# Performance work log

Hardware: AMD Instinct MI355X
Metric: run time of the kernel (lower is better)

## Reference

```python
import jax, jax.numpy as jnp
import numpy as np

N_ATOMS = 100000   # real atoms (index 0 is padding row -> total rows N_ATOMS+1)
N_BONDS = 200000   # real directed bonds (index 0 is padding row)
MAX_NB = 6
HIDDEN = 300
ATOM_FDIM = 133
BOND_FDIM = 147
DEPTH = 3
N_MOLS = 5000
ATOMS_PER_MOL = N_ATOMS // N_MOLS


def setup_inputs() -> dict:
    key = jax.random.key(0)
    ks = jax.random.split(key, 8)
    f_atoms = jax.random.normal(ks[0], (N_ATOMS + 1, ATOM_FDIM), dtype=jnp.float32)
    f_atoms = f_atoms.at[0].set(0.0)  # chemprop zero-padding row
    f_bonds = jax.random.normal(ks[1], (N_BONDS + 1, BOND_FDIM), dtype=jnp.float32)
    f_bonds = f_bonds.at[0].set(0.0)
    # weights (Linear stored as [in, out]); bias=False for W_i/W_h, W_o has bias
    W_i = jax.random.normal(ks[2], (BOND_FDIM, HIDDEN), dtype=jnp.float32) * 0.05
    W_h = jax.random.normal(ks[3], (HIDDEN, HIDDEN), dtype=jnp.float32) * 0.05
    W_o = jax.random.normal(ks[4], (ATOM_FDIM + HIDDEN, HIDDEN), dtype=jnp.float32) * 0.05
    b_o = jnp.zeros((HIDDEN,), dtype=jnp.float32)
    # a2b: incoming bond ids per atom, padded with 0 (padding row of message is 0)
    a2b = jax.random.randint(ks[5], (N_ATOMS + 1, MAX_NB), 0, N_BONDS + 1, dtype=jnp.int32)
    a2b = a2b.at[0].set(0)
    # b2a: source atom of each bond
    b2a = jax.random.randint(ks[6], (N_BONDS + 1,), 1, N_ATOMS + 1, dtype=jnp.int32)
    b2a = b2a.at[0].set(0)
    # b2revb: reverse-bond pairing; bonds (2k+1, 2k+2) are partners, 0 -> 0
    idx = jnp.arange(N_BONDS + 1, dtype=jnp.int32)
    b2revb = jnp.where(idx == 0, 0, ((idx - 1) ^ 1) + 1).astype(jnp.int32)
    # molecule segment id for each real atom (replaces a_scope loop)
    mol_ids = (jnp.arange(N_ATOMS, dtype=jnp.int32) // ATOMS_PER_MOL).astype(jnp.int32)
    return {"f_atoms": f_atoms, "f_bonds": f_bonds, "W_i": W_i, "W_h": W_h,
            "W_o": W_o, "b_o": b_o, "a2b": a2b, "b2a": b2a, "b2revb": b2revb,
            "mol_ids": mol_ids}


def reference(f_atoms, f_bonds, W_i, W_h, W_o, b_o, a2b, b2a, b2revb, mol_ids):
    # input = act(W_i(f_bonds))  (ReLU, bias=False)
    inp = jax.nn.relu(f_bonds @ W_i)                    # [B+1, H]
    message = inp
    for _ in range(DEPTH - 1):
        nei = message[a2b]                              # [A+1, MAX_NB, H] gather
        a_message = nei.sum(axis=1)                     # [A+1, H]
        message = a_message[b2a] - message[b2revb]      # [B+1, H]
        message = jax.nn.relu(inp + message @ W_h)      # skip-connection + act
    # final atom readout
    a_message = message[a2b].sum(axis=1)                # [A+1, H]
    a_input = jnp.concatenate([f_atoms, a_message], axis=1)
    atom_hiddens = jax.nn.relu(a_input @ W_o + b_o)     # [A+1, H]
    # per-molecule mean pooling over real atoms (rows 1:)
    real = atom_hiddens[1:]                             # [A, H]
    sums = jax.ops.segment_sum(real, mol_ids, num_segments=N_MOLS)
    counts = jax.ops.segment_sum(jnp.ones((N_ATOMS,), dtype=real.dtype), mol_ids,
                                 num_segments=N_MOLS)
    mol_vecs = sums / jnp.maximum(counts, 1.0)[:, None]  # [N_MOLS, H]
    return mol_vecs
```

## Files before the change

### kernel.cpp

```cpp
#include <hip/hip_runtime.h>
#include <hip/hip_bf16.h>

#define N_ATOMS   100000
#define N_BONDS   200000
#define MAX_NB    6
#define HIDDEN    300
#define ATOM_FDIM 133
#define BOND_FDIM 147
#define N_MOLS    5000
#define APM       20

#define MB_ROWS (N_BONDS + 1)
#define MA_ROWS (N_ATOMS + 1)

#define CHUNKS_B 1280
#define EPS      308

typedef unsigned short bf16_t;
typedef __attribute__((ext_vector_type(8))) __bf16 bf16x8;
typedef __attribute__((ext_vector_type(4))) float  float4v;

__device__ __forceinline__ float bf2f(unsigned short u) {
    union { unsigned int i; float f; } x; x.i = ((unsigned int)u) << 16; return x.f;
}
__device__ __forceinline__ unsigned short f2bf(float f) {
    union { float f; unsigned int i; } x; x.f = f;
    unsigned int r = x.i + 0x7FFFu + ((x.i >> 16) & 1u);
    return (unsigned short)(r >> 16);
}

__global__ __launch_bounds__(256) void prep_w(
    const float* __restrict__ W, bf16_t* __restrict__ dst, int K, int total_chunks)
{
    int idx = blockIdx.x * 256 + threadIdx.x;
    if (idx >= total_chunks) return;
    int kb  = idx / CHUNKS_B;
    int c   = idx - kb * CHUNKS_B;
    int cq  = c / 320;
    int col = c - cq * 320;
    unsigned short v[8];
    #pragma unroll
    for (int j = 0; j < 8; ++j) {
        int k = kb * 32 + cq * 8 + j;
        float f = (k < K && col < HIDDEN) ? W[(size_t)k * HIDDEN + col] : 0.f;
        v[j] = f2bf(f);
    }
    bf16_t* p = dst + (size_t)idx * 8;
    *(ushort4*)(p)     = make_ushort4(v[0], v[1], v[2], v[3]);
    *(ushort4*)(p + 4) = make_ushort4(v[4], v[5], v[6], v[7]);
}

template<int MODE, int KB>
__global__ __launch_bounds__(512, 4) void gemm_mfma(
    const float* __restrict__ Af,
    const bf16_t* __restrict__ Ab1, const bf16_t* __restrict__ Ab2,
    const int* __restrict__ b2a, const int* __restrict__ b2revb,
    const bf16_t* __restrict__ WB, const float* __restrict__ bias,
    const bf16_t* __restrict__ addend, bf16_t* __restrict__ Y,
    int M)
{
    const int S = HIDDEN;
    constexpr int QG = KB * 4;
    constexpr int LDS_BYTES = (KB * 4096 > 16 * EPS * 4) ? KB * 4096 : 16 * EPS * 4;
    __shared__ __align__(16) char lds_pool[LDS_BYTES];
    bf16_t* As  = (bf16_t*)lds_pool;
    float*  epi = (float*)lds_pool;
    __shared__ int rowmap[128];

    const int tid  = threadIdx.x;
    const int lane = tid & 63;
    const int w    = tid >> 6;
    const int wm   = w >> 2;
    const int wn   = w & 3;
    const int lrow = lane & 15;
    const int q    = lane >> 4;
    const int bm   = blockIdx.x * 64;

    if (MODE == 1) {
        if (tid < 64) {
            int sr = bm + tid;
            rowmap[tid] = (sr < M) ? b2a[sr] : 0;
        } else if (tid < 128) {
            int sr = bm + tid - 64;
            rowmap[tid] = (sr < M) ? b2revb[sr] : 0;
        }
        __syncthreads();
    }

    for (int t = tid; t < 64 * QG; t += 512) {
        int row = t / QG;
        int qg  = t - row * QG;
        int k0  = qg * 8;
        unsigned short av[8];
        if (MODE == 1) {
            const bf16_t* pa = Ab1 + (size_t)rowmap[row]      * S;
            const bf16_t* pc = Ab2 + (size_t)rowmap[64 + row] * S;
            if (k0 + 8 <= S) {
                ushort4 a0 = *(const ushort4*)(pa + k0);
                ushort4 a1 = *(const ushort4*)(pa + k0 + 4);
                ushort4 c0 = *(const ushort4*)(pc + k0);
                ushort4 c1 = *(const ushort4*)(pc + k0 + 4);
                av[0] = f2bf(bf2f(a0.x) - bf2f(c0.x));
                av[1] = f2bf(bf2f(a0.y) - bf2f(c0.y));
                av[2] = f2bf(bf2f(a0.z) - bf2f(c0.z));
                av[3] = f2bf(bf2f(a0.w) - bf2f(c0.w));
                av[4] = f2bf(bf2f(a1.x) - bf2f(c1.x));
                av[5] = f2bf(bf2f(a1.y) - bf2f(c1.y));
                av[6] = f2bf(bf2f(a1.z) - bf2f(c1.z));
                av[7] = f2bf(bf2f(a1.w) - bf2f(c1.w));
            } else {
                #pragma unroll
                for (int j = 0; j < 8; ++j) {
                    int k = k0 + j;
                    av[j] = (k < S) ? f2bf(bf2f(pa[k]) - bf2f(pc[k]))
                                    : (unsigned short)0;
                }
            }
        } else if (MODE == 0) {
            int srow = bm + row;
            #pragma unroll
            for (int j = 0; j < 8; ++j) {
                int k = k0 + j;
                av[j] = (srow < M && k < BOND_FDIM)
                        ? f2bf(Af[(size_t)srow * BOND_FDIM + k]) : (unsigned short)0;
            }
        } else {
            int srow = bm + row;
            #pragma unroll
            for (int j = 0; j < 8; ++j) {
                int k = k0 + j;
                unsigned short u = 0;
                if (srow < M) {
                    if (k < ATOM_FDIM)
                        u = f2bf(Af[(size_t)srow * ATOM_FDIM + k]);
                    else if (k < ATOM_FDIM + HIDDEN)
                        u = Ab1[(size_t)srow * S + (k - ATOM_FDIM)];
                }
                av[j] = u;
            }
        }
        bf16_t* dst = As + (size_t)(qg * 64 + row) * 8;
        *(ushort4*)(dst)     = make_ushort4(av[0], av[1], av[2], av[3]);
        *(ushort4*)(dst + 4) = make_ushort4(av[4], av[5], av[6], av[7]);
    }

    float4v acc[2][5];
    #pragma unroll
    for (int i = 0; i < 2; ++i)
        #pragma unroll
        for (int j = 0; j < 5; ++j) {
            float4v z = {0.f, 0.f, 0.f, 0.f};
            acc[i][j] = z;
        }

    __syncthreads();

    const bf16_t* wbase = WB + (size_t)(q * 320 + wn * 80 + lrow) * 8;
    #pragma unroll 2
    for (int kb = 0; kb < KB; ++kb) {
        bf16x8 af0 = *(const bf16x8*)(As + (size_t)((kb * 4 + q) * 64 + wm * 32 + lrow) * 8);
        bf16x8 af1 = *(const bf16x8*)(As + (size_t)((kb * 4 + q) * 64 + wm * 32 + 16 + lrow) * 8);
        const bf16_t* wk = wbase + (size_t)kb * (CHUNKS_B * 8);
        #pragma unroll
        for (int nt = 0; nt < 5; ++nt) {
            const int c0 = wn * 80 + nt * 16;
            if (c0 < HIDDEN) {
                bf16x8 bfr = *(const bf16x8*)(wk + (size_t)nt * 16 * 8);
                acc[0][nt] = __builtin_amdgcn_mfma_f32_16x16x32_bf16(af0, bfr, acc[0][nt], 0, 0, 0);
                acc[1][nt] = __builtin_amdgcn_mfma_f32_16x16x32_bf16(af1, bfr, acc[1][nt], 0, 0, 0);
            }
        }
    }

    __syncthreads();
    #pragma unroll
    for (int mt = 0; mt < 2; ++mt) {
        for (int wh = 0; wh < 2; ++wh) {
            if (wm == wh) {
                #pragma unroll
                for (int nt = 0; nt < 5; ++nt) {
                    const int c0 = wn * 80 + nt * 16;
                    if (c0 < HIDDEN) {
                        #pragma unroll
                        for (int r = 0; r < 4; ++r)
                            epi[(q * 4 + r) * EPS + c0 + lrow] = acc[mt][nt][r];
                    }
                }
            }
            __syncthreads();
            const int row0 = bm + wh * 32 + mt * 16;
            for (int s = tid; s < 16 * 75; s += 512) {
                int rr = s / 75;
                int c4 = s - rr * 75;
                int grow = row0 + rr;
                if (grow < M) {
                    float4 v = *(const float4*)&epi[rr * EPS + c4 * 4];
                    if (MODE == 1) {
                        ushort4 ad = *(const ushort4*)(addend + (size_t)grow * S + c4 * 4);
                        v.x += bf2f(ad.x); v.y += bf2f(ad.y);
                        v.z += bf2f(ad.z); v.w += bf2f(ad.w);
                    }
                    if (MODE == 2) {
                        float4 bv = *(const float4*)(bias + c4 * 4);
                        v.x += bv.x; v.y += bv.y; v.z += bv.z; v.w += bv.w;
                    }
                    ushort4 o;
                    o.x = f2bf(v.x > 0.f ? v.x : 0.f);
                    o.y = f2bf(v.y > 0.f ? v.y : 0.f);
                    o.z = f2bf(v.z > 0.f ? v.z : 0.f);
                    o.w = f2bf(v.w > 0.f ? v.w : 0.f);
                    *(ushort4*)(Y + (size_t)grow * S + c4 * 4) = o;
                }
            }
            __syncthreads();
        }
    }
}


__global__ __launch_bounds__(256) void aggregate_k(
    const bf16_t* __restrict__ msg, const int* __restrict__ a2b,
    bf16_t* __restrict__ amsg)
{
    int idx = blockIdx.x * blockDim.x + threadIdx.x;
    const int total = MA_ROWS * 75;
    if (idx >= total) return;
    int a  = idx / 75;
    int c4 = idx - a * 75;
    const int* nb = a2b + (size_t)a * MAX_NB;
    float4 s = make_float4(0.f, 0.f, 0.f, 0.f);
    #pragma unroll
    for (int j = 0; j < MAX_NB; ++j) {
        int b = nb[j];
        ushort4 u = *(const ushort4*)(msg + (size_t)b * HIDDEN + c4 * 4);
        s.x += bf2f(u.x); s.y += bf2f(u.y); s.z += bf2f(u.z); s.w += bf2f(u.w);
    }
    ushort4 o;
    o.x = f2bf(s.x); o.y = f2bf(s.y); o.z = f2bf(s.z); o.w = f2bf(s.w);
    *(ushort4*)(amsg + (size_t)a * HIDDEN + c4 * 4) = o;
}

__global__ __launch_bounds__(256) void mol_mean_k(
    const bf16_t* __restrict__ atom_h, float* __restrict__ out)
{
    int idx = blockIdx.x * blockDim.x + threadIdx.x;
    if (idx >= N_MOLS * 75) return;
    int m  = idx / 75;
    int c4 = idx - m * 75;
    const bf16_t* base = atom_h + (size_t)(1 + m * APM) * HIDDEN + c4 * 4;
    float4 s = make_float4(0.f, 0.f, 0.f, 0.f);
    #pragma unroll
    for (int i = 0; i < APM; ++i) {
        ushort4 u = *(const ushort4*)(base + (size_t)i * HIDDEN);
        s.x += bf2f(u.x); s.y += bf2f(u.y); s.z += bf2f(u.z); s.w += bf2f(u.w);
    }
    const float inv = 1.0f / (float)APM;
    s.x *= inv; s.y *= inv; s.z *= inv; s.w *= inv;
    *(float4*)(out + (size_t)m * HIDDEN + c4 * 4) = s;
}

extern "C" void kernel_launch(void* const* d_in, const int* in_sizes, int n_in,
                              void* d_out, int out_size, void* d_ws, size_t ws_size,
                              hipStream_t stream)
{
    const float* f_atoms = (const float*)d_in[0];
    const float* f_bonds = (const float*)d_in[1];
    const float* W_i     = (const float*)d_in[2];
    const float* W_h     = (const float*)d_in[3];
    const float* W_o     = (const float*)d_in[4];
    const float* b_o     = (const float*)d_in[5];
    const int*   a2b     = (const int*)d_in[6];
    const int*   b2a     = (const int*)d_in[7];
    const int*   b2revb  = (const int*)d_in[8];
    float* out = (float*)d_out;

    char* base = (char*)d_ws;
    const size_t SZ_BOND_B = (((size_t)MB_ROWS * HIDDEN * sizeof(bf16_t)) + 255) & ~(size_t)255;
    bf16_t* inp  = (bf16_t*)(base);
    bf16_t* msgA = (bf16_t*)(base + SZ_BOND_B);
    bf16_t* amsg = (bf16_t*)(base + 2 * SZ_BOND_B);

    char* scratch = (char*)d_out;
    bf16_t* Wib = (bf16_t*)(scratch);
    bf16_t* Whb = (bf16_t*)(scratch + 102400);
    bf16_t* Wob = (bf16_t*)(scratch + 307200);

    dim3 blk512(512), blk256(256);
    const int gb = (MB_ROWS + 63) / 64;
    const int ga = (MA_ROWS + 63) / 64;
    int agg_blocks  = (MA_ROWS * 75 + 255) / 256;
    int mean_blocks = (N_MOLS * 75 + 255) / 256;

    prep_w<<<(5  * CHUNKS_B + 255) / 256, blk256, 0, stream>>>(W_i, Wib, BOND_FDIM, 5 * CHUNKS_B);
    prep_w<<<(10 * CHUNKS_B + 255) / 256, blk256, 0, stream>>>(W_h, Whb, HIDDEN, 10 * CHUNKS_B);
    prep_w<<<(14 * CHUNKS_B + 255) / 256, blk256, 0, stream>>>(W_o, Wob, ATOM_FDIM + HIDDEN, 14 * CHUNKS_B);

    gemm_mfma<0, 5><<<gb, blk512, 0, stream>>>(
        f_bonds, nullptr, nullptr, nullptr, nullptr,
        Wib, nullptr, nullptr, inp, MB_ROWS);

    aggregate_k<<<agg_blocks, blk256, 0, stream>>>(inp, a2b, amsg);
    gemm_mfma<1, 10><<<gb, blk512, 0, stream>>>(
        nullptr, amsg, inp, b2a, b2revb,
        Whb, nullptr, inp, msgA, MB_ROWS);

    aggregate_k<<<agg_blocks, blk256, 0, stream>>>(msgA, a2b, amsg);
    gemm_mfma<1, 10><<<gb, blk512, 0, stream>>>(
        nullptr, amsg, msgA, b2a, b2revb,
        Whb, nullptr, inp, inp, MB_ROWS);

    aggregate_k<<<agg_blocks, blk256, 0, stream>>>(inp, a2b, amsg);
    gemm_mfma<2, 14><<<ga, blk512, 0, stream>>>(
        f_atoms, amsg, nullptr, nullptr, nullptr,
        Wob, b_o, nullptr, msgA, MA_ROWS);

    mol_mean_k<<<mean_blocks, blk256, 0, stream>>>(msgA, out);
}
```

Before: 947.1 us.

## Batch gathers, pad LDS rows, prefetch weight fragments, widen aggregate per thread

The A-tile staging now issues all global loads into registers before converting and storing them to LDS, so more gathers are in flight at once. LDS rows are padded to 65 to cut bank conflicts. The MFMA loop is fully unrolled and double-buffers the B fragments from global memory. W_o is K-permuted so atom features align to 136, which lets the readout GEMM load message columns as vector chunks. The aggregate kernel now handles 12 columns per thread with all neighbor loads issued up front. The price is higher register pressure under launch_bounds(512,4), which could cause spills.

```diff
diff --git a/kernel.cpp b/kernel.cpp
--- a/kernel.cpp
+++ b/kernel.cpp
@@ -15,6 +15,7 @@
 
 #define CHUNKS_B 1280
 #define EPS      308
+#define ROWP     65
 
 typedef unsigned short bf16_t;
 typedef __attribute__((ext_vector_type(8))) __bf16 bf16x8;
@@ -30,7 +31,8 @@
 }
 
 __global__ __launch_bounds__(256) void prep_w(
-    const float* __restrict__ W, bf16_t* __restrict__ dst, int K, int total_chunks)
+    const float* __restrict__ W, bf16_t* __restrict__ dst, int K,
+    int total_chunks, int perm)
 {
     int idx = blockIdx.x * 256 + threadIdx.x;
     if (idx >= total_chunks) return;
@@ -42,7 +44,10 @@
     #pragma unroll
     for (int j = 0; j < 8; ++j) {
         int k = kb * 32 + cq * 8 + j;
-        float f = (k < K && col < HIDDEN) ? W[(size_t)k * HIDDEN + col] : 0.f;
+        int ksrc;
+        if (perm) ksrc = (k < 133) ? k : ((k >= 136 && k < 436) ? k - 3 : -1);
+        else      ksrc = (k < K) ? k : -1;
+        float f = (ksrc >= 0 && col < HIDDEN) ? W[(size_t)ksrc * HIDDEN + col] : 0.f;
         v[j] = f2bf(f);
     }
     bf16_t* p = dst + (size_t)idx * 8;
@@ -61,7 +66,9 @@
 {
     const int S = HIDDEN;
     constexpr int QG = KB * 4;
-    constexpr int LDS_BYTES = (KB * 4096 > 16 * EPS * 4) ? KB * 4096 : 16 * EPS * 4;
+    constexpr int NT = (64 * QG + 511) / 512;
+    constexpr int ASZ = QG * ROWP * 16;
+    constexpr int LDS_BYTES = (ASZ > 16 * EPS * 4) ? ASZ : 16 * EPS * 4;
     __shared__ __align__(16) char lds_pool[LDS_BYTES];
     bf16_t* As  = (bf16_t*)lds_pool;
     float*  epi = (float*)lds_pool;
@@ -87,61 +94,90 @@
         __syncthreads();
     }
 
-    for (int t = tid; t < 64 * QG; t += 512) {
-        int row = t / QG;
-        int qg  = t - row * QG;
-        int k0  = qg * 8;
-        unsigned short av[8];
-        if (MODE == 1) {
-            const bf16_t* pa = Ab1 + (size_t)rowmap[row]      * S;
-            const bf16_t* pc = Ab2 + (size_t)rowmap[64 + row] * S;
-            if (k0 + 8 <= S) {
-                ushort4 a0 = *(const ushort4*)(pa + k0);
-                ushort4 a1 = *(const ushort4*)(pa + k0 + 4);
-                ushort4 c0 = *(const ushort4*)(pc + k0);
-                ushort4 c1 = *(const ushort4*)(pc + k0 + 4);
-                av[0] = f2bf(bf2f(a0.x) - bf2f(c0.x));
-                av[1] = f2bf(bf2f(a0.y) - bf2f(c0.y));
-                av[2] = f2bf(bf2f(a0.z) - bf2f(c0.z));
-                av[3] = f2bf(bf2f(a0.w) - bf2f(c0.w));
-                av[4] = f2bf(bf2f(a1.x) - bf2f(c1.x));
-                av[5] = f2bf(bf2f(a1.y) - bf2f(c1.y));
-                av[6] = f2bf(bf2f(a1.z) - bf2f(c1.z));
-                av[7] = f2bf(bf2f(a1.w) - bf2f(c1.w));
-            } else {
+    ushort4 A0[NT], A1[NT], C0[NT], C1[NT];
+    float   F[(MODE == 1) ? 1 : NT][8];
+    const ushort4 zz = make_ushort4(0, 0, 0, 0);
+
+    #pragma unroll
+    for (int i = 0; i < NT; ++i) {
+        int t = tid + i * 512;
+        if (t < 64 * QG) {
+            int row = t / QG;
+            int qg  = t - row * QG;
+            int k0  = qg * 8;
+            if (MODE == 1) {
+                const bf16_t* pa = Ab1 + (size_t)rowmap[row]      * S;
+                const bf16_t* pc = Ab2 + (size_t)rowmap[64 + row] * S;
+                A0[i] = (k0 + 4 <= S) ? *(const ushort4*)(pa + k0)     : zz;
+                A1[i] = (k0 + 8 <= S) ? *(const ushort4*)(pa + k0 + 4) : zz;
+                C0[i] = (k0 + 4 <= S) ? *(const ushort4*)(pc + k0)     : zz;
+                C1[i] = (k0 + 8 <= S) ? *(const ushort4*)(pc + k0 + 4) : zz;
+            } else if (MODE == 0) {
+                int srow = bm + row;
                 #pragma unroll
                 for (int j = 0; j < 8; ++j) {
                     int k = k0 + j;
-                    av[j] = (k < S) ? f2bf(bf2f(pa[k]) - bf2f(pc[k]))
-                                    : (unsigned short)0;
-                }
-            }
-        } else if (MODE == 0) {
-            int srow = bm + row;
-            #pragma unroll
-            for (int j = 0; j < 8; ++j) {
-                int k = k0 + j;
-                av[j] = (srow < M && k < BOND_FDIM)
-                        ? f2bf(Af[(size_t)srow * BOND_FDIM + k]) : (unsigned short)0;
-            }
-        } else {
-            int srow = bm + row;
-            #pragma unroll
-            for (int j = 0; j < 8; ++j) {
-                int k = k0 + j;
-                unsigned short u = 0;
-                if (srow < M) {
-                    if (k < ATOM_FDIM)
-                        u = f2bf(Af[(size_t)srow * ATOM_FDIM + k]);
-                    else if (k < ATOM_FDIM + HIDDEN)
-                        u = Ab1[(size_t)srow * S + (k - ATOM_FDIM)];
-                }
-                av[j] = u;
-            }
-        }
-        bf16_t* dst = As + (size_t)(qg * 64 + row) * 8;
-        *(ushort4*)(dst)     = make_ushort4(av[0], av[1], av[2], av[3]);
-        *(ushort4*)(dst + 4) = make_ushort4(av[4], av[5], av[6], av[7]);
+                    F[i][j] = (srow < M && k < BOND_FDIM)
+                              ? Af[(size_t)srow * BOND_FDIM + k] : 0.f;
+                }
+            } else {
+                int srow = bm + row;
+                if (k0 < 136) {
+                    #pragma unroll
+                    for (int j = 0; j < 8; ++j) {
+                        int k = k0 + j;
+                        F[i][j] = (srow < M && k < ATOM_FDIM)
+                                  ? Af[(size_t)srow * ATOM_FDIM + k] : 0.f;
+                    }
+                } else {
+                    int off = k0 - 136;
+                    const bf16_t* pm = Ab1 + (size_t)srow * S;
+                    ushort4 u0 = (srow < M && off + 4 <= S)
+                                 ? *(const ushort4*)(pm + off)     : zz;
+                    ushort4 u1 = (srow < M && off + 8 <= S)
+                                 ? *(const ushort4*)(pm + off + 4) : zz;
+                    *(ushort4*)&F[i][0] = u0;
+                    *(ushort4*)&F[i][2] = u1;
+                }
+            }
+        }
+    }
+
+    #pragma unroll
+    for (int i = 0; i < NT; ++i) {
+        int t = tid + i * 512;
+        if (t < 64 * QG) {
+            int row = t / QG;
+            int qg  = t - row * QG;
+            unsigned short av[8];
+            if (MODE == 1) {
+                av[0] = f2bf(bf2f(A0[i].x) - bf2f(C0[i].x));
+                av[1] = f2bf(bf2f(A0[i].y) - bf2f(C0[i].y));
+                av[2] = f2bf(bf2f(A0[i].z) - bf2f(C0[i].z));
+                av[3] = f2bf(bf2f(A0[i].w) - bf2f(C0[i].w));
+                av[4] = f2bf(bf2f(A1[i].x) - bf2f(C1[i].x));
+                av[5] = f2bf(bf2f(A1[i].y) - bf2f(C1[i].y));
+                av[6] = f2bf(bf2f(A1[i].z) - bf2f(C1[i].z));
+                av[7] = f2bf(bf2f(A1[i].w) - bf2f(C1[i].w));
+            } else if (MODE == 0) {
+                #pragma unroll
+                for (int j = 0; j < 8; ++j) av[j] = f2bf(F[i][j]);
+            } else {
+                int k0 = qg * 8;
+                if (k0 < 136) {
+                    #pragma unroll
+                    for (int j = 0; j < 8; ++j) av[j] = f2bf(F[i][j]);
+                } else {
+                    ushort4 u0 = *(const ushort4*)&F[i][0];
+                    ushort4 u1 = *(const ushort4*)&F[i][2];
+                    av[0] = u0.x; av[1] = u0.y; av[2] = u0.z; av[3] = u0.w;
+                    av[4] = u1.x; av[5] = u1.y; av[6] = u1.z; av[7] = u1.w;
+                }
+            }
+            bf16_t* dst = As + (size_t)(qg * ROWP + row) * 8;
+            *(ushort4*)(dst)     = make_ushort4(av[0], av[1], av[2], av[3]);
+            *(ushort4*)(dst + 4) = make_ushort4(av[4], av[5], av[6], av[7]);
+        }
     }
 
     float4v acc[2][5];
@@ -155,20 +191,33 @@
 
     __syncthreads();
 
-    const bf16_t* wbase = WB + (size_t)(q * 320 + wn * 80 + lrow) * 8;
-    #pragma unroll 2
+    const bf16_t* wptr = WB + (size_t)(q * 320 + wn * 80 + lrow) * 8;
+    bf16x8 bcur[5], bnxt[5];
+    #pragma unroll
+    for (int nt = 0; nt < 5; ++nt)
+        bcur[nt] = *(const bf16x8*)(wptr + nt * 128);
+
+    #pragma unroll
     for (int kb = 0; kb < KB; ++kb) {
-        bf16x8 af0 = *(const bf16x8*)(As + (size_t)((kb * 4 + q) * 64 + wm * 32 + lrow) * 8);
-        bf16x8 af1 = *(const bf16x8*)(As + (size_t)((kb * 4 + q) * 64 + wm * 32 + 16 + lrow) * 8);
-        const bf16_t* wk = wbase + (size_t)kb * (CHUNKS_B * 8);
+        const bf16_t* abase = As + (size_t)((kb * 4 + q) * ROWP + wm * 32 + lrow) * 8;
+        bf16x8 af0 = *(const bf16x8*)(abase);
+        bf16x8 af1 = *(const bf16x8*)(abase + 16 * 8);
+        if (kb + 1 < KB) {
+            const bf16_t* wnx = wptr + (size_t)(kb + 1) * (CHUNKS_B * 8);
+            #pragma unroll
+            for (int nt = 0; nt < 5; ++nt)
+                bnxt[nt] = *(const bf16x8*)(wnx + nt * 128);
+        }
         #pragma unroll
         for (int nt = 0; nt < 5; ++nt) {
-            const int c0 = wn * 80 + nt * 16;
-            if (c0 < HIDDEN) {
-                bf16x8 bfr = *(const bf16x8*)(wk + (size_t)nt * 16 * 8);
-                acc[0][nt] = __builtin_amdgcn_mfma_f32_16x16x32_bf16(af0, bfr, acc[0][nt], 0, 0, 0);
-                acc[1][nt] = __builtin_amdgcn_mfma_f32_16x16x32_bf16(af1, bfr, acc[1][nt], 0, 0, 0);
-            }
+            if (wn * 80 + nt * 16 < HIDDEN) {
+                acc[0][nt] = __builtin_amdgcn_mfma_f32_16x16x32_bf16(af0, bcur[nt], acc[0][nt], 0, 0, 0);
+                acc[1][nt] = __builtin_amdgcn_mfma_f32_16x16x32_bf16(af1, bcur[nt], acc[1][nt], 0, 0, 0);
+            }
+        }
+        if (kb + 1 < KB) {
+            #pragma unroll
+            for (int nt = 0; nt < 5; ++nt) bcur[nt] = bnxt[nt];
         }
     }
 
@@ -217,27 +266,44 @@
     }
 }
 
-
 __global__ __launch_bounds__(256) void aggregate_k(
     const bf16_t* __restrict__ msg, const int* __restrict__ a2b,
     bf16_t* __restrict__ amsg)
 {
     int idx = blockIdx.x * blockDim.x + threadIdx.x;
-    const int total = MA_ROWS * 75;
+    const int total = MA_ROWS * 25;
     if (idx >= total) return;
-    int a  = idx / 75;
-    int c4 = idx - a * 75;
+    int a  = idx / 25;
+    int g  = idx - a * 25;
+    int c0 = g * 12;
     const int* nb = a2b + (size_t)a * MAX_NB;
-    float4 s = make_float4(0.f, 0.f, 0.f, 0.f);
+    int b[MAX_NB];
+    #pragma unroll
+    for (int j = 0; j < MAX_NB; ++j) b[j] = nb[j];
+    ushort4 u0[MAX_NB], u1[MAX_NB], u2[MAX_NB];
     #pragma unroll
     for (int j = 0; j < MAX_NB; ++j) {
-        int b = nb[j];
-        ushort4 u = *(const ushort4*)(msg + (size_t)b * HIDDEN + c4 * 4);
-        s.x += bf2f(u.x); s.y += bf2f(u.y); s.z += bf2f(u.z); s.w += bf2f(u.w);
-    }
-    ushort4 o;
-    o.x = f2bf(s.x); o.y = f2bf(s.y); o.z = f2bf(s.z); o.w = f2bf(s.w);
-    *(ushort4*)(amsg + (size_t)a * HIDDEN + c4 * 4) = o;
+        const bf16_t* p = msg + (size_t)b[j] * HIDDEN + c0;
+        u0[j] = *(const ushort4*)(p);
+        u1[j] = *(const ushort4*)(p + 4);
+        u2[j] = *(const ushort4*)(p + 8);
+    }
+    float s[12];
+    #pragma unroll
+    for (int k = 0; k < 12; ++k) s[k] = 0.f;
+    #pragma unroll
+    for (int j = 0; j < MAX_NB; ++j) {
+        s[0] += bf2f(u0[j].x); s[1]  += bf2f(u0[j].y);
+        s[2] += bf2f(u0[j].z); s[3]  += bf2f(u0[j].w);
+        s[4] += bf2f(u1[j].x); s[5]  += bf2f(u1[j].y);
+        s[6] += bf2f(u1[j].z); s[7]  += bf2f(u1[j].w);
+        s[8] += bf2f(u2[j].x); s[9]  += bf2f(u2[j].y);
+        s[10]+= bf2f(u2[j].z); s[11] += bf2f(u2[j].w);
+    }
+    bf16_t* o = amsg + (size_t)a * HIDDEN + c0;
+    *(ushort4*)(o)     = make_ushort4(f2bf(s[0]), f2bf(s[1]), f2bf(s[2]),  f2bf(s[3]));
+    *(ushort4*)(o + 4) = make_ushort4(f2bf(s[4]), f2bf(s[5]), f2bf(s[6]),  f2bf(s[7]));
+    *(ushort4*)(o + 8) = make_ushort4(f2bf(s[8]), f2bf(s[9]), f2bf(s[10]), f2bf(s[11]));
 }
 
 __global__ __launch_bounds__(256) void mol_mean_k(
@@ -288,12 +354,12 @@
     dim3 blk512(512), blk256(256);
     const int gb = (MB_ROWS + 63) / 64;
     const int ga = (MA_ROWS + 63) / 64;
-    int agg_blocks  = (MA_ROWS * 75 + 255) / 256;
+    int agg_blocks  = (MA_ROWS * 25 + 255) / 256;
     int mean_blocks = (N_MOLS * 75 + 255) / 256;
 
-    prep_w<<<(5  * CHUNKS_B + 255) / 256, blk256, 0, stream>>>(W_i, Wib, BOND_FDIM, 5 * CHUNKS_B);
-    prep_w<<<(10 * CHUNKS_B + 255) / 256, blk256, 0, stream>>>(W_h, Whb, HIDDEN, 10 * CHUNKS_B);
-    prep_w<<<(14 * CHUNKS_B + 255) / 256, blk256, 0, stream>>>(W_o, Wob, ATOM_FDIM + HIDDEN, 14 * CHUNKS_B);
+    prep_w<<<(5  * CHUNKS_B + 255) / 256, blk256, 0, stream>>>(W_i, Wib, BOND_FDIM, 5 * CHUNKS_B, 0);
+    prep_w<<<(10 * CHUNKS_B + 255) / 256, blk256, 0, stream>>>(W_h, Whb, HIDDEN, 10 * CHUNKS_B, 0);
+    prep_w<<<(14 * CHUNKS_B + 255) / 256, blk256, 0, stream>>>(W_o, Wob, 436, 14 * CHUNKS_B, 1);
 
     gemm_mfma<0, 5><<<gb, blk512, 0, stream>>>(
         f_bonds, nullptr, nullptr, nullptr, nullptr,
```

New measurement: 849.4 us. 10.3% less time.
